# Optimization experiments

Hardware: AMD Instinct MI355X
Metric: run time of the kernel (lower is better)

Reference implementation:

```python
import jax, jax.numpy as jnp
import numpy as np


def _mlp(x, W0, b0, W1, b1, W2, b2, W3, b3):
    # 4-layer MLP, ReLU between layers, no final activation
    h = jax.nn.relu(x @ W0 + b0)
    h = jax.nn.relu(h @ W1 + b1)
    h = jax.nn.relu(h @ W2 + b2)
    return h @ W3 + b3


def setup_inputs() -> dict:
    key = jax.random.key(0)
    ks = jax.random.split(key, 8)
    B, t, p, f = 4, 12, 32, 64          # num_graphs, timesteps, n_patches, nhid
    n = 10000                            # nodes per graph
    E = 200000                           # subgraph-node membership entries
    in_dim = f * t + t                   # 780
    horizon = 12
    scale = 0.02
    return {
        "mixer_x": jax.random.normal(ks[0], (B, t, p, f), jnp.float32),
        "features": jax.random.normal(ks[1], (B * n, t), jnp.float32),
        "subgraphs_batch": jax.random.randint(ks[2], (E,), 0, p * B),
        "subgraphs_nodes_mapper": jax.random.randint(ks[3], (E,), 0, n * B),
        "W0": jax.random.normal(ks[4], (in_dim, in_dim), jnp.float32) * scale,
        "b0": jnp.zeros((in_dim,), jnp.float32),
        "W1": jax.random.normal(ks[5], (in_dim, in_dim), jnp.float32) * scale,
        "b1": jnp.zeros((in_dim,), jnp.float32),
        "W2": jax.random.normal(ks[6], (in_dim, in_dim), jnp.float32) * scale,
        "b2": jnp.zeros((in_dim,), jnp.float32),
        "W3": jax.random.normal(ks[7], (in_dim, horizon), jnp.float32) * scale,
        "b3": jnp.zeros((horizon,), jnp.float32),
    }


def reference(mixer_x, features, subgraphs_batch, subgraphs_nodes_mapper,
              W0, b0, W1, b1, W2, b2, W3, b3):
    B, t, p, f = mixer_x.shape
    n_seg = features.shape[0]                      # n * B segments
    n = n_seg // B
    # passthrough: '(B n) t -> B n t'
    passthrough = features.reshape(B, n, t)
    # mixer_x: 'B t p f -> (p B) t f'
    flat = jnp.transpose(mixer_x, (2, 0, 1, 3)).reshape(p * B, t, f)
    # gather by subgraph index, then scatter-mean over node mapper
    gathered = flat[subgraphs_batch]               # (E, t, f)
    sums = jax.ops.segment_sum(gathered, subgraphs_nodes_mapper, num_segments=n_seg)
    counts = jax.ops.segment_sum(jnp.ones((gathered.shape[0],), gathered.dtype),
                                 subgraphs_nodes_mapper, num_segments=n_seg)
    nodes = sums / jnp.maximum(counts, 1.0)[:, None, None]   # (n*B, t, f)
    # '(n B) t f -> B n (t f)'
    nodes = jnp.transpose(nodes.reshape(n, B, t, f), (1, 0, 2, 3)).reshape(B, n, t * f)
    mlp_in = jnp.concatenate([passthrough, nodes], axis=-1)  # (B, n, t + t*f)
    mlp_out = _mlp(mlp_in, W0, b0, W1, b1, W2, b2, W3, b3)   # (B, n, horizon)
    # 'B n h -> (B n) h'
    return mlp_out.reshape(B * n, -1)
```

## Files before the change

kernel.cpp:

```cpp
#include <hip/hip_runtime.h>

#define BG    4
#define TT    12
#define NN    10000
#define EN    200000
#define NSEG  40000
#define NROWS 40000
#define MPAD  40064
#define KD    832
#define KA0   160
#define NPW   896
#define NT    7

typedef __attribute__((ext_vector_type(8))) short bf8_t;
typedef __attribute__((ext_vector_type(4))) float f4_t;

__device__ __forceinline__ unsigned short f2bf(float x) {
  unsigned int u = __float_as_uint(x);
  u += 0x7fffu + ((u >> 16) & 1u);
  return (unsigned short)(u >> 16);
}

#define GLDS16(src, dst) __builtin_amdgcn_global_load_lds( \
    (const __attribute__((address_space(1))) void*)(src),  \
    (__attribute__((address_space(3))) void*)(dst), 16, 0, 0)

#define LKW0 asm volatile("s_waitcnt lgkmcnt(0)" ::: "memory")
#define VMW0 asm volatile("s_waitcnt vmcnt(0)" ::: "memory")

__global__ void k_zero(int* counts) {
  int i = blockIdx.x * 256 + threadIdx.x;
  if (i < NSEG) counts[i] = 0;
}

__global__ void k_count(const int* __restrict__ mapper, int* __restrict__ counts) {
  int e = blockIdx.x * 256 + threadIdx.x;
  if (e < EN) atomicAdd(&counts[mapper[e]], 1);
}

__global__ void k_zerof(float* __restrict__ p, int n) {
  int i = blockIdx.x * 256 + threadIdx.x;
  if (i < n) p[i] = 0.f;
}

__global__ void k_scatterCf(const int* __restrict__ mapper, const int* __restrict__ batch,
                            float* __restrict__ Cff) {
  int e = blockIdx.x * 256 + threadIdx.x;
  if (e < EN) {
    const int s = mapper[e];
    const int r = (s % BG) * NN + s / BG;
    atomicAdd(&Cff[(size_t)r * 128 + batch[e]], 1.0f);
  }
}

__global__ void k_buildA(const float* __restrict__ features, const int* __restrict__ counts,
                         const float* __restrict__ Cff, unsigned short* __restrict__ A) {
  int idx = blockIdx.x * 256 + threadIdx.x;
  if (idx >= MPAD * KA0) return;
  const int r = idx / KA0, c = idx - r * KA0;
  float v = 0.f;
  if (r < NROWS) {
    if (c < 12) {
      v = features[(size_t)r * TT + c];
    } else if (c < 140) {
      const int s = (r % NN) * BG + (r / NN);
      const int cnt = counts[s];
      const float inv = 1.f / (float)(cnt > 0 ? cnt : 1);
      v = Cff[(size_t)r * 128 + (c - 12)] * inv;
    }
  }
  A[idx] = f2bf(v);
}

__global__ void k_buildB(const float* __restrict__ W0, const float* __restrict__ fW0,
                         unsigned short* __restrict__ WTB) {
  int idx = blockIdx.x * 256 + threadIdx.x;
  if (idx >= NPW * KA0) return;
  const int n = idx / KA0, k = idx - n * KA0;
  float v = 0.f;
  if (n < 780) {
    if (k < 12) v = W0[(size_t)k * 780 + n];
    else if (k < 140) v = fW0[(size_t)(k - 12) * KD + n];
  }
  WTB[idx] = f2bf(v);
}

__global__ void k_tpad(const float* __restrict__ W, unsigned short* __restrict__ Wt,
                       int ldw, int nsrc, int total) {
  int idx = blockIdx.x * 256 + threadIdx.x;
  if (idx >= total) return;
  int n = idx / KD, k = idx % KD;
  float v = (n < nsrc && k < 780) ? W[k * ldw + n] : 0.f;
  Wt[idx] = f2bf(v);
}

__global__ void k_padbias3(const float* __restrict__ b0, const float* __restrict__ b1,
                           const float* __restrict__ b2, float* __restrict__ p0,
                           float* __restrict__ p1, float* __restrict__ p2) {
  int i = blockIdx.x * 256 + threadIdx.x;
  if (i >= 3 * KD) return;
  const int which = i / KD, c = i - which * KD;
  const float* src = which == 0 ? b0 : (which == 1 ? b1 : b2);
  float* dst = which == 0 ? p0 : (which == 1 ? p1 : p2);
  dst[c] = (c < 780) ? src[c] : 0.f;
}

__global__ __launch_bounds__(256) void k_flatW0(const float* __restrict__ mixer,
                                                const float* __restrict__ W0,
                                                float* __restrict__ fW0) {
  __shared__ float sA[8][768];
  __shared__ float sRed[4][64][9];
  const int tid = threadIdx.x;
  const int c0 = blockIdx.x * 64, j0 = blockIdx.y * 8;
  for (int i = tid; i < 8 * 768; i += 256) {
    int jj = i / 768;
    int k = i - jj * 768;
    int j = j0 + jj;
    int tt = k >> 6, ff = k & 63;
    sA[jj][k] = mixer[(((j & 3) * TT + tt) * 32 + (j >> 2)) * 64 + ff];
  }
  __syncthreads();
  const int cc = tid & 63, ks = tid >> 6;
  const int c = c0 + cc;
  float acc[8] = {};
  if (c < 780) {
    const float* wp = W0 + (size_t)(12 + ks * 192) * 780 + c;
    #pragma unroll 4
    for (int k = ks * 192; k < ks * 192 + 192; ++k) {
      const float w = *wp; wp += 780;
      #pragma unroll
      for (int jj = 0; jj < 8; ++jj) acc[jj] = fmaf(sA[jj][k], w, acc[jj]);
    }
  }
  #pragma unroll
  for (int jj = 0; jj < 8; ++jj) sRed[ks][cc][jj] = acc[jj];
  __syncthreads();
  for (int o = tid; o < 512; o += 256) {
    const int oc = o & 63, jj = o >> 6;
    const int wc = c0 + oc;
    if (wc < KD) {
      float s = sRed[0][oc][jj] + sRed[1][oc][jj] + sRed[2][oc][jj] + sRed[3][oc][jj];
      fW0[(size_t)(j0 + jj) * KD + wc] = s;
    }
  }
}

template<int KA, int BK>
__global__ __launch_bounds__(256) void gemm_relu(
    const unsigned short* __restrict__ A, const unsigned short* __restrict__ WT,
    const float* __restrict__ bias, unsigned short* __restrict__ C) {
  constexpr int SEGR = BK / 8;
  constexpr int MASK = SEGR - 1;
  constexpr int NISS = (128 * SEGR) / 256;
  constexpr int NKT  = KA / BK;
  constexpr int NKK  = BK / 32;
  __shared__ unsigned short sA[2][128 * BK];
  __shared__ unsigned short sB[2][128 * BK];
  const int tid = threadIdx.x, lane = tid & 63, wid = tid >> 6;
  const int wm = wid >> 1, wn = wid & 1;

  const int nwg = gridDim.x;
  const int q = nwg >> 3, r8 = nwg & 7;
  const int xcd = blockIdx.x & 7, bidx = blockIdx.x >> 3;
  const int linear = (xcd < r8 ? xcd * (q + 1) : r8 * (q + 1) + (xcd - r8) * q) + bidx;
  const int rowtile = linear / NT, ntile = linear - rowtile * NT;

  const int row0 = rowtile * 128, n0 = ntile * 128;
  const char* gA = (const char*)A + (size_t)row0 * (KA * 2);
  const char* gB = (const char*)WT + (size_t)n0 * (KA * 2);
  const int frow = lane & 15;

  int offA[NKK][4], offB[NKK][4];
  #pragma unroll
  for (int kk = 0; kk < NKK; ++kk) {
    const int c16r = kk * 4 + (lane >> 4);
    #pragma unroll
    for (int i = 0; i < 4; ++i) {
      const int ra = wm * 64 + i * 16 + frow;
      const int rb = wn * 64 + i * 16 + frow;
      offA[kk][i] = ra * BK + ((c16r ^ (ra & MASK)) * 8);
      offB[kk][i] = rb * BK + ((c16r ^ (rb & MASK)) * 8);
    }
  }

  auto stage = [&](int b, int kt) {
    const int kb = kt * (BK * 2);
    #pragma unroll
    for (int L = 0; L < NISS; ++L) {
      const int seg = L * 256 + wid * 64 + lane;
      const int row = seg / SEGR, c16 = seg & MASK;
      const int c16s = c16 ^ (row & MASK);
      const size_t go = (size_t)row * (KA * 2) + kb + c16s * 16;
      GLDS16(gA + go, (char*)sA[b] + seg * 16);
      GLDS16(gB + go, (char*)sB[b] + seg * 16);
    }
  };

  f4_t acc[4][4] = {};

  stage(0, 0);
  stage(1, 1);
  if constexpr (BK == 64) asm volatile("s_waitcnt vmcnt(8)" ::: "memory");
  else                    asm volatile("s_waitcnt vmcnt(4)" ::: "memory");
  __builtin_amdgcn_s_barrier();

  #pragma unroll
  for (int t = 0; t < NKT; ++t) {
    const int cur = t & 1;
    bf8_t af[NKK][4], bfv[NKK][4];
    #pragma unroll
    for (int kk = 0; kk < NKK; ++kk) {
      #pragma unroll
      for (int i = 0; i < 4; ++i) {
        af[kk][i]  = *(const bf8_t*)(&sA[cur][offA[kk][i]]);
        bfv[kk][i] = *(const bf8_t*)(&sB[cur][offB[kk][i]]);
      }
    }
    if (t < NKT - 1) {
      LKW0;
      __builtin_amdgcn_s_barrier();
      __builtin_amdgcn_sched_barrier(0);
      if (t + 2 < NKT) stage(cur, t + 2);
    }
    __builtin_amdgcn_s_setprio(1);
    #pragma unroll
    for (int kk = 0; kk < NKK; ++kk)
      #pragma unroll
      for (int mi = 0; mi < 4; ++mi)
        #pragma unroll
        for (int ni = 0; ni < 4; ++ni)
          acc[mi][ni] = __builtin_amdgcn_mfma_f32_16x16x32_bf16(bfv[kk][ni], af[kk][mi], acc[mi][ni], 0, 0, 0);
    __builtin_amdgcn_s_setprio(0);
    if (t < NKT - 1) {
      if (t + 2 < NKT) {
        if constexpr (BK == 64) asm volatile("s_waitcnt vmcnt(8)" ::: "memory");
        else                    asm volatile("s_waitcnt vmcnt(4)" ::: "memory");
      } else {
        VMW0;
      }
      __builtin_amdgcn_s_barrier();
    }
  }

  const int cq = (lane >> 4) * 4;
  #pragma unroll
  for (int mi = 0; mi < 4; ++mi) {
    const int r = row0 + wm * 64 + mi * 16 + frow;
    unsigned short* crow = C + (size_t)r * KD;
    #pragma unroll
    for (int ni = 0; ni < 4; ++ni) {
      const int c = n0 + wn * 64 + ni * 16 + cq;
      if (c < KD) {
        f4_t v = acc[mi][ni];
        const f4_t bb = *(const f4_t*)(bias + c);
        float v0 = fmaxf(v[0] + bb[0], 0.f);
        float v1 = fmaxf(v[1] + bb[1], 0.f);
        float v2 = fmaxf(v[2] + bb[2], 0.f);
        float v3 = fmaxf(v[3] + bb[3], 0.f);
        uint2 pk;
        pk.x = (unsigned int)f2bf(v0) | ((unsigned int)f2bf(v1) << 16);
        pk.y = (unsigned int)f2bf(v2) | ((unsigned int)f2bf(v3) << 16);
        *(uint2*)(crow + c) = pk;
      }
    }
  }
}

__global__ __launch_bounds__(256) void gemm_out(
    const unsigned short* __restrict__ A, const unsigned short* __restrict__ WT3,
    const float* __restrict__ b3, float* __restrict__ out) {
  __shared__ unsigned short sA[128 * 64];
  __shared__ unsigned short sB[16 * 64];
  const int tid = threadIdx.x, lane = tid & 63, wid = tid >> 6;
  const int row0 = blockIdx.x * 128;
  const char* gA = (const char*)A + (size_t)row0 * (KD * 2);
  const char* gB = (const char*)WT3;
  const int frow = lane & 15, fk = (lane >> 4) * 8;

  f4_t acc[2] = {};

  for (int kt = 0; kt < KD / 64; ++kt) {
    const int kb = kt * 128;
    __syncthreads();
    #pragma unroll
    for (int L = 0; L < 4; ++L) {
      const int seg = L * 256 + wid * 64 + lane;
      const int row = seg >> 3, c16 = seg & 7;
      GLDS16(gA + (size_t)row * (KD * 2) + kb + c16 * 16, (char*)sA + seg * 16);
    }
    if (wid == 0) {
      #pragma unroll
      for (int L = 0; L < 2; ++L) {
        const int seg = L * 64 + lane;
        const int row = seg >> 3, c16 = seg & 7;
        GLDS16(gB + (size_t)row * (KD * 2) + kb + c16 * 16, (char*)sB + seg * 16);
      }
    }
    __syncthreads();
    #pragma unroll
    for (int kk = 0; kk < 2; ++kk) {
      const bf8_t bf = *(const bf8_t*)(&sB[frow * 64 + kk * 32 + fk]);
      #pragma unroll
      for (int mi = 0; mi < 2; ++mi) {
        const bf8_t af = *(const bf8_t*)(&sA[(wid * 32 + mi * 16 + frow) * 64 + kk * 32 + fk]);
        acc[mi] = __builtin_amdgcn_mfma_f32_16x16x32_bf16(bf, af, acc[mi], 0, 0, 0);
      }
    }
  }

  const int cg = (lane >> 4) * 4;
  #pragma unroll
  for (int mi = 0; mi < 2; ++mi) {
    const int r = row0 + wid * 32 + mi * 16 + frow;
    if (r < NROWS && cg < 12) {
      f4_t v = acc[mi];
      const f4_t bb = *(const f4_t*)(b3 + cg);
      v += bb;
      *(f4_t*)(out + (size_t)r * 12 + cg) = v;
    }
  }
}

extern "C" void kernel_launch(void* const* d_in, const int* in_sizes, int n_in,
                              void* d_out, int out_size, void* d_ws, size_t ws_size,
                              hipStream_t stream) {
  const float* mixer    = (const float*)d_in[0];
  const float* features = (const float*)d_in[1];
  const int*   sg_batch = (const int*)d_in[2];
  const int*   sg_map   = (const int*)d_in[3];
  const float* W0 = (const float*)d_in[4];  const float* b0 = (const float*)d_in[5];
  const float* W1 = (const float*)d_in[6];  const float* b1 = (const float*)d_in[7];
  const float* W2 = (const float*)d_in[8];  const float* b2 = (const float*)d_in[9];
  const float* W3 = (const float*)d_in[10]; const float* b3 = (const float*)d_in[11];
  float* out = (float*)d_out;

  char* wsp = (char*)d_ws;
  auto alloc = [&](size_t bytes) { char* p = wsp; wsp += (bytes + 255) & ~(size_t)255; return p; };
  unsigned short* h0  = (unsigned short*)alloc((size_t)MPAD * KD * 2);
  unsigned short* h1  = (unsigned short*)alloc((size_t)MPAD * KD * 2);
  unsigned short* Wt1 = (unsigned short*)alloc((size_t)NPW * KD * 2);
  unsigned short* Wt2 = (unsigned short*)alloc((size_t)NPW * KD * 2);
  unsigned short* Wt3 = (unsigned short*)alloc((size_t)16 * KD * 2);
  unsigned short* WTB = (unsigned short*)alloc((size_t)NPW * KA0 * 2);
  float* bp0   = (float*)alloc(KD * 4);
  float* bp1   = (float*)alloc(KD * 4);
  float* bp2   = (float*)alloc(KD * 4);
  float* fW0   = (float*)alloc((size_t)128 * KD * 4);
  int* counts  = (int*)alloc(NSEG * 4);
  float* Cff = (float*)h1;
  unsigned short* Abuf = (unsigned short*)((char*)h1 + ((size_t)MPAD * 128 * 4 + 255 & ~(size_t)255));

  k_zero<<<(NSEG + 255) / 256, 256, 0, stream>>>(counts);
  k_count<<<(EN + 255) / 256, 256, 0, stream>>>(sg_map, counts);

  k_zerof<<<(MPAD * 128 + 255) / 256, 256, 0, stream>>>(Cff, MPAD * 128);
  k_scatterCf<<<(EN + 255) / 256, 256, 0, stream>>>(sg_map, sg_batch, Cff);

  k_flatW0<<<dim3(13, 16), 256, 0, stream>>>(mixer, W0, fW0);
  k_tpad<<<(NPW * KD + 255) / 256, 256, 0, stream>>>(W1, Wt1, 780, 780, NPW * KD);
  k_tpad<<<(NPW * KD + 255) / 256, 256, 0, stream>>>(W2, Wt2, 780, 780, NPW * KD);
  k_tpad<<<(16 * KD + 255) / 256, 256, 0, stream>>>(W3, Wt3, 12, 12, 16 * KD);
  k_padbias3<<<(3 * KD + 255) / 256, 256, 0, stream>>>(b0, b1, b2, bp0, bp1, bp2);
  k_buildB<<<(NPW * KA0 + 255) / 256, 256, 0, stream>>>(W0, fW0, WTB);

  k_buildA<<<(MPAD * KA0 + 255) / 256, 256, 0, stream>>>(features, counts, Cff, Abuf);

  gemm_relu<KA0, 32><<<(MPAD / 128) * NT, 256, 0, stream>>>(Abuf, WTB, bp0, h0);

  gemm_relu<KD, 64><<<(MPAD / 128) * NT, 256, 0, stream>>>(h0, Wt1, bp1, h1);
  gemm_relu<KD, 64><<<(MPAD / 128) * NT, 256, 0, stream>>>(h1, Wt2, bp2, h0);

  gemm_out<<<MPAD / 128, 256, 0, stream>>>(h0, Wt3, b3, out);
}
```

Baseline: 359.9 us.

## Fuse final output layer into last ReLU GEMM epilogue and merge prep kernels

The last hidden-layer GEMM now keeps its ReLU'd bf16 tile in swizzled shared memory and multiplies it by the matching slice of W3 on the spot. Each column tile atomically adds its partial 12-wide output into a buffer pre-initialised with b3. This removes the separate output GEMM and the write and re-read of the final hidden activation. Zeroing, weight transpose/padding and bias padding kernels are merged into fewer launches. The cost is seven float atomics per output element and extra epilogue LDS work, and the summation order becomes nondeterministic.

```diff
diff --git a/kernel.cpp b/kernel.cpp
--- a/kernel.cpp
+++ b/kernel.cpp
@@ -11,6 +11,7 @@
 #define KA0   160
 #define NPW   896
 #define NT    7
+#define KW3   896
 
 typedef __attribute__((ext_vector_type(8))) short bf8_t;
 typedef __attribute__((ext_vector_type(4))) float f4_t;
@@ -27,20 +28,19 @@
 
 #define LKW0 asm volatile("s_waitcnt lgkmcnt(0)" ::: "memory")
 #define VMW0 asm volatile("s_waitcnt vmcnt(0)" ::: "memory")
-
-__global__ void k_zero(int* counts) {
+#define SBAR0 __builtin_amdgcn_sched_barrier(0)
+
+__global__ void k_init(int* __restrict__ counts, float* __restrict__ Cff,
+                       float* __restrict__ out3, const float* __restrict__ b3) {
   int i = blockIdx.x * 256 + threadIdx.x;
   if (i < NSEG) counts[i] = 0;
+  if (i < MPAD * 128) Cff[i] = 0.f;
+  if (i < NROWS * 12) out3[i] = b3[i % 12];
 }
 
 __global__ void k_count(const int* __restrict__ mapper, int* __restrict__ counts) {
   int e = blockIdx.x * 256 + threadIdx.x;
   if (e < EN) atomicAdd(&counts[mapper[e]], 1);
-}
-
-__global__ void k_zerof(float* __restrict__ p, int n) {
-  int i = blockIdx.x * 256 + threadIdx.x;
-  if (i < n) p[i] = 0.f;
 }
 
 __global__ void k_scatterCf(const int* __restrict__ mapper, const int* __restrict__ batch,
@@ -72,37 +72,53 @@
   A[idx] = f2bf(v);
 }
 
-__global__ void k_buildB(const float* __restrict__ W0, const float* __restrict__ fW0,
-                         unsigned short* __restrict__ WTB) {
+__global__ void k_prep(const float* __restrict__ W0, const float* __restrict__ fW0,
+                       const float* __restrict__ W1, const float* __restrict__ W2,
+                       const float* __restrict__ W3,
+                       const float* __restrict__ b0, const float* __restrict__ b1,
+                       const float* __restrict__ b2,
+                       unsigned short* __restrict__ Wt1, unsigned short* __restrict__ Wt2,
+                       unsigned short* __restrict__ Wt3,
+                       float* __restrict__ bp0, float* __restrict__ bp1,
+                       float* __restrict__ bp2, unsigned short* __restrict__ WTB) {
+  constexpr int S1 = NPW * KD;
+  constexpr int S3 = 16 * KW3;
+  constexpr int SB = 3 * NPW;
+  constexpr int S5 = NPW * KA0;
   int idx = blockIdx.x * 256 + threadIdx.x;
-  if (idx >= NPW * KA0) return;
-  const int n = idx / KA0, k = idx - n * KA0;
-  float v = 0.f;
-  if (n < 780) {
-    if (k < 12) v = W0[(size_t)k * 780 + n];
-    else if (k < 140) v = fW0[(size_t)(k - 12) * KD + n];
-  }
-  WTB[idx] = f2bf(v);
-}
-
-__global__ void k_tpad(const float* __restrict__ W, unsigned short* __restrict__ Wt,
-                       int ldw, int nsrc, int total) {
-  int idx = blockIdx.x * 256 + threadIdx.x;
-  if (idx >= total) return;
-  int n = idx / KD, k = idx % KD;
-  float v = (n < nsrc && k < 780) ? W[k * ldw + n] : 0.f;
-  Wt[idx] = f2bf(v);
-}
-
-__global__ void k_padbias3(const float* __restrict__ b0, const float* __restrict__ b1,
-                           const float* __restrict__ b2, float* __restrict__ p0,
-                           float* __restrict__ p1, float* __restrict__ p2) {
-  int i = blockIdx.x * 256 + threadIdx.x;
-  if (i >= 3 * KD) return;
-  const int which = i / KD, c = i - which * KD;
-  const float* src = which == 0 ? b0 : (which == 1 ? b1 : b2);
-  float* dst = which == 0 ? p0 : (which == 1 ? p1 : p2);
-  dst[c] = (c < 780) ? src[c] : 0.f;
+  if (idx < 2 * S1) {
+    const int which = idx / S1, rem = idx - which * S1;
+    const int n = rem / KD, k = rem - n * KD;
+    const float* W = which ? W2 : W1;
+    float v = (n < 780 && k < 780) ? W[(size_t)k * 780 + n] : 0.f;
+    (which ? Wt2 : Wt1)[rem] = f2bf(v);
+    return;
+  }
+  idx -= 2 * S1;
+  if (idx < S3) {
+    const int n = idx / KW3, k = idx - n * KW3;
+    float v = (n < 12 && k < 780) ? W3[(size_t)k * 12 + n] : 0.f;
+    Wt3[idx] = f2bf(v);
+    return;
+  }
+  idx -= S3;
+  if (idx < SB) {
+    const int which = idx / NPW, c = idx - which * NPW;
+    const float* src = which == 0 ? b0 : (which == 1 ? b1 : b2);
+    float* dst = which == 0 ? bp0 : (which == 1 ? bp1 : bp2);
+    dst[c] = (c < 780) ? src[c] : 0.f;
+    return;
+  }
+  idx -= SB;
+  if (idx < S5) {
+    const int n = idx / KA0, k = idx - n * KA0;
+    float v = 0.f;
+    if (n < 780) {
+      if (k < 12) v = W0[(size_t)k * 780 + n];
+      else if (k < 140) v = fW0[(size_t)(k - 12) * KD + n];
+    }
+    WTB[idx] = f2bf(v);
+  }
 }
 
 __global__ __launch_bounds__(256) void k_flatW0(const float* __restrict__ mixer,
@@ -145,10 +161,11 @@
   }
 }
 
-template<int KA, int BK>
+template<int KA, int BK, bool FUSE>
 __global__ __launch_bounds__(256) void gemm_relu(
     const unsigned short* __restrict__ A, const unsigned short* __restrict__ WT,
-    const float* __restrict__ bias, unsigned short* __restrict__ C) {
+    const float* __restrict__ bias, unsigned short* __restrict__ C,
+    const unsigned short* __restrict__ W3t, float* __restrict__ out3) {
   constexpr int SEGR = BK / 8;
   constexpr int MASK = SEGR - 1;
   constexpr int NISS = (128 * SEGR) / 256;
@@ -219,7 +236,7 @@
     if (t < NKT - 1) {
       LKW0;
       __builtin_amdgcn_s_barrier();
-      __builtin_amdgcn_sched_barrier(0);
+      SBAR0;
       if (t + 2 < NKT) stage(cur, t + 2);
     }
     __builtin_amdgcn_s_setprio(1);
@@ -243,16 +260,39 @@
   }
 
   const int cq = (lane >> 4) * 4;
-  #pragma unroll
-  for (int mi = 0; mi < 4; ++mi) {
-    const int r = row0 + wm * 64 + mi * 16 + frow;
-    unsigned short* crow = C + (size_t)r * KD;
-    #pragma unroll
-    for (int ni = 0; ni < 4; ++ni) {
-      const int c = n0 + wn * 64 + ni * 16 + cq;
-      if (c < KD) {
+  if constexpr (!FUSE) {
+    #pragma unroll
+    for (int mi = 0; mi < 4; ++mi) {
+      const int r = row0 + wm * 64 + mi * 16 + frow;
+      unsigned short* crow = C + (size_t)r * KD;
+      #pragma unroll
+      for (int ni = 0; ni < 4; ++ni) {
+        const int c = n0 + wn * 64 + ni * 16 + cq;
+        if (c < KD) {
+          f4_t v = acc[mi][ni];
+          const f4_t bb = *(const f4_t*)(bias + c);
+          float v0 = fmaxf(v[0] + bb[0], 0.f);
+          float v1 = fmaxf(v[1] + bb[1], 0.f);
+          float v2 = fmaxf(v[2] + bb[2], 0.f);
+          float v3 = fmaxf(v[3] + bb[3], 0.f);
+          uint2 pk;
+          pk.x = (unsigned int)f2bf(v0) | ((unsigned int)f2bf(v1) << 16);
+          pk.y = (unsigned int)f2bf(v2) | ((unsigned int)f2bf(v3) << 16);
+          *(uint2*)(crow + c) = pk;
+        }
+      }
+    }
+  } else {
+    unsigned short* sT = (unsigned short*)sA;
+    __syncthreads();
+    #pragma unroll
+    for (int mi = 0; mi < 4; ++mi) {
+      const int lr = wm * 64 + mi * 16 + frow;
+      #pragma unroll
+      for (int ni = 0; ni < 4; ++ni) {
+        const int lc = wn * 64 + ni * 16 + cq;
         f4_t v = acc[mi][ni];
-        const f4_t bb = *(const f4_t*)(bias + c);
+        const f4_t bb = *(const f4_t*)(bias + (n0 + lc));
         float v0 = fmaxf(v[0] + bb[0], 0.f);
         float v1 = fmaxf(v[1] + bb[1], 0.f);
         float v2 = fmaxf(v[2] + bb[2], 0.f);
@@ -260,63 +300,34 @@
         uint2 pk;
         pk.x = (unsigned int)f2bf(v0) | ((unsigned int)f2bf(v1) << 16);
         pk.y = (unsigned int)f2bf(v2) | ((unsigned int)f2bf(v3) << 16);
-        *(uint2*)(crow + c) = pk;
-      }
-    }
-  }
-}
-
-__global__ __launch_bounds__(256) void gemm_out(
-    const unsigned short* __restrict__ A, const unsigned short* __restrict__ WT3,
-    const float* __restrict__ b3, float* __restrict__ out) {
-  __shared__ unsigned short sA[128 * 64];
-  __shared__ unsigned short sB[16 * 64];
-  const int tid = threadIdx.x, lane = tid & 63, wid = tid >> 6;
-  const int row0 = blockIdx.x * 128;
-  const char* gA = (const char*)A + (size_t)row0 * (KD * 2);
-  const char* gB = (const char*)WT3;
-  const int frow = lane & 15, fk = (lane >> 4) * 8;
-
-  f4_t acc[2] = {};
-
-  for (int kt = 0; kt < KD / 64; ++kt) {
-    const int kb = kt * 128;
+        const int bo = (lr * 256 + lc * 2) ^ ((lr & 7) << 4);
+        *(uint2*)((char*)sT + bo) = pk;
+      }
+    }
     __syncthreads();
-    #pragma unroll
-    for (int L = 0; L < 4; ++L) {
-      const int seg = L * 256 + wid * 64 + lane;
-      const int row = seg >> 3, c16 = seg & 7;
-      GLDS16(gA + (size_t)row * (KD * 2) + kb + c16 * 16, (char*)sA + seg * 16);
-    }
-    if (wid == 0) {
-      #pragma unroll
-      for (int L = 0; L < 2; ++L) {
-        const int seg = L * 64 + lane;
-        const int row = seg >> 3, c16 = seg & 7;
-        GLDS16(gB + (size_t)row * (KD * 2) + kb + c16 * 16, (char*)sB + seg * 16);
-      }
-    }
-    __syncthreads();
-    #pragma unroll
-    for (int kk = 0; kk < 2; ++kk) {
-      const bf8_t bf = *(const bf8_t*)(&sB[frow * 64 + kk * 32 + fk]);
-      #pragma unroll
-      for (int mi = 0; mi < 2; ++mi) {
-        const bf8_t af = *(const bf8_t*)(&sA[(wid * 32 + mi * 16 + frow) * 64 + kk * 32 + fk]);
-        acc[mi] = __builtin_amdgcn_mfma_f32_16x16x32_bf16(bf, af, acc[mi], 0, 0, 0);
-      }
-    }
-  }
-
-  const int cg = (lane >> 4) * 4;
-  #pragma unroll
-  for (int mi = 0; mi < 2; ++mi) {
-    const int r = row0 + wid * 32 + mi * 16 + frow;
-    if (r < NROWS && cg < 12) {
-      f4_t v = acc[mi];
-      const f4_t bb = *(const f4_t*)(b3 + cg);
-      v += bb;
-      *(f4_t*)(out + (size_t)r * 12 + cg) = v;
+    const int fk = (lane >> 4) * 8;
+    f4_t acc2[2] = {};
+    #pragma unroll
+    for (int kk2 = 0; kk2 < 4; ++kk2) {
+      const bf8_t bw = *(const bf8_t*)(W3t + (size_t)frow * KW3 + n0 + kk2 * 32 + fk);
+      #pragma unroll
+      for (int mi2 = 0; mi2 < 2; ++mi2) {
+        const int lr2 = wid * 32 + mi2 * 16 + frow;
+        const int bo = (lr2 * 256 + (kk2 * 32 + fk) * 2) ^ ((lr2 & 7) << 4);
+        const bf8_t av = *(const bf8_t*)((char*)sT + bo);
+        acc2[mi2] = __builtin_amdgcn_mfma_f32_16x16x32_bf16(bw, av, acc2[mi2], 0, 0, 0);
+      }
+    }
+    #pragma unroll
+    for (int mi2 = 0; mi2 < 2; ++mi2) {
+      const int r2 = row0 + wid * 32 + mi2 * 16 + frow;
+      if (r2 < NROWS && cq < 12) {
+        float* orow = out3 + (size_t)r2 * 12 + cq;
+        atomicAdd(&orow[0], acc2[mi2][0]);
+        atomicAdd(&orow[1], acc2[mi2][1]);
+        atomicAdd(&orow[2], acc2[mi2][2]);
+        atomicAdd(&orow[3], acc2[mi2][3]);
+      }
     }
   }
 }
@@ -340,35 +351,32 @@
   unsigned short* h1  = (unsigned short*)alloc((size_t)MPAD * KD * 2);
   unsigned short* Wt1 = (unsigned short*)alloc((size_t)NPW * KD * 2);
   unsigned short* Wt2 = (unsigned short*)alloc((size_t)NPW * KD * 2);
-  unsigned short* Wt3 = (unsigned short*)alloc((size_t)16 * KD * 2);
+  unsigned short* Wt3 = (unsigned short*)alloc((size_t)16 * KW3 * 2);
   unsigned short* WTB = (unsigned short*)alloc((size_t)NPW * KA0 * 2);
-  float* bp0   = (float*)alloc(KD * 4);
-  float* bp1   = (float*)alloc(KD * 4);
-  float* bp2   = (float*)alloc(KD * 4);
+  float* bp0   = (float*)alloc(NPW * 4);
+  float* bp1   = (float*)alloc(NPW * 4);
+  float* bp2   = (float*)alloc(NPW * 4);
   float* fW0   = (float*)alloc((size_t)128 * KD * 4);
   int* counts  = (int*)alloc(NSEG * 4);
   float* Cff = (float*)h1;
   unsigned short* Abuf = (unsigned short*)((char*)h1 + ((size_t)MPAD * 128 * 4 + 255 & ~(size_t)255));
 
-  k_zero<<<(NSEG + 255) / 256, 256, 0, stream>>>(counts);
+  k_init<<<(MPAD * 128 + 255) / 256, 256, 0, stream>>>(counts, Cff, out, b3);
   k_count<<<(EN + 255) / 256, 256, 0, stream>>>(sg_map, counts);
-
-  k_zerof<<<(MPAD * 128 + 255) / 256, 256, 0, stream>>>(Cff, MPAD * 128);
   k_scatterCf<<<(EN + 255) / 256, 256, 0, stream>>>(sg_map, sg_batch, Cff);
 
   k_flatW0<<<dim3(13, 16), 256, 0, stream>>>(mixer, W0, fW0);
-  k_tpad<<<(NPW * KD + 255) / 256, 256, 0, stream>>>(W1, Wt1, 780, 780, NPW * KD);
-  k_tpad<<<(NPW * KD + 255) / 256, 256, 0, stream>>>(W2, Wt2, 780, 780, NPW * KD);
-  k_tpad<<<(16 * KD + 255) / 256, 256, 0, stream>>>(W3, Wt3, 12, 12, 16 * KD);
-  k_padbias3<<<(3 * KD + 255) / 256, 256, 0, stream>>>(b0, b1, b2, bp0, bp1, bp2);
-  k_buildB<<<(NPW * KA0 + 255) / 256, 256, 0, stream>>>(W0, fW0, WTB);
+  {
+    const int total = 2 * (NPW * KD) + 16 * KW3 + 3 * NPW + NPW * KA0;
+    k_prep<<<(total + 255) / 256, 256, 0, stream>>>(W0, fW0, W1, W2, W3, b0, b1, b2,
+                                                    Wt1, Wt2, Wt3, bp0, bp1, bp2, WTB);
+  }
 
   k_buildA<<<(MPAD * KA0 + 255) / 256, 256, 0, stream>>>(features, counts, Cff, Abuf);
 
-  gemm_relu<KA0, 32><<<(MPAD / 128) * NT, 256, 0, stream>>>(Abuf, WTB, bp0, h0);
-
-  gemm_relu<KD, 64><<<(MPAD / 128) * NT, 256, 0, stream>>>(h0, Wt1, bp1, h1);
-  gemm_relu<KD, 64><<<(MPAD / 128) * NT, 256, 0, stream>>>(h1, Wt2, bp2, h0);
-
-  gemm_out<<<MPAD / 128, 256, 0, stream>>>(h0, Wt3, b3, out);
-}
+  gemm_relu<KA0, 32, false><<<(MPAD / 128) * NT, 256, 0, stream>>>(Abuf, WTB, bp0, h0, nullptr, nullptr);
+
+  gemm_relu<KD, 64, false><<<(MPAD / 128) * NT, 256, 0, stream>>>(h0, Wt1, bp1, h1, nullptr, nullptr);
+
+  gemm_relu<KD, 64, true><<<(MPAD / 128) * NT, 256, 0, stream>>>(h1, Wt2, bp2, nullptr, Wt3, out);
+}
```

Result: faster. 347.0 us (-3.6%).
